# Kernel optimization log

Measured on AMD Instinct MI355X. Metric: run time of the kernel, lower is better.

The kernel has to match this reference:

```python
import jax, jax.numpy as jnp
import numpy as np
import math

M = 4096   # mem_dim == hidden_size (required: C @ qt)
D = 2048   # input_size


def setup_inputs() -> dict:
    key = jax.random.key(0)
    ks = jax.random.split(key, 16)
    f = lambda k, s: jax.random.normal(k, s, dtype=jnp.float32)
    return {
        "x": f(ks[0], (D, 1)),
        "cp": f(ks[1], (M, M)),
        "n_prev": f(ks[2], (M, 1)),
        "Wq": f(ks[3], (M, D)),
        "bq": f(ks[4], (M, 1)),
        "Wk": f(ks[5], (M, D)),
        "bk": f(ks[6], (M, 1)),
        "Wv": f(ks[7], (M, D)),
        "bV": f(ks[8], (M, 1)),
        "Wi": f(ks[9], (1, D)),
        "bi": f(ks[10], (1,)),
        "Wf": f(ks[11], (1, D)),
        "bf": f(ks[12], (1,)),
        "Wo": f(ks[13], (1, D)),
        "bo": f(ks[14], (1,)),
    }


def reference(x, cp, n_prev, Wq, bq, Wk, bk, Wv, bV, Wi, bi, Wf, bf, Wo, bo):
    inv_sqrt_m = 1.0 / math.sqrt(M)
    qt = Wq @ x + bq                      # (M, 1)
    kt = inv_sqrt_m * (Wk @ x + bk)       # (M, 1)
    vt = Wv @ x + bV                      # (M, 1)
    it = jnp.exp(Wi @ x + bi)             # (1, 1) input gate (exp)
    ft = jnp.exp(Wf @ x + bf)             # (1, 1) forget gate (exp)
    v = vt[:, 0]                          # (M,)
    k = kt[:, 0]                          # (M,)
    # matrix memory update: C = f*C_prev + i * v k^T
    C = ft * cp + it * jnp.outer(v, k)    # (M, M)
    n = ft * n_prev + it * k[:, None]     # (M, 1)
    denom = jnp.maximum(jnp.abs(n.T @ qt), 1.0)   # (1, 1)
    h_tilde = (C @ qt) / denom            # (M, 1)
    ot = jax.nn.sigmoid(Wo @ x + bo)      # (1, 1)
    ht = ot * h_tilde                     # (M, 1)
    return (ht, C, n)
```

## Files before the change

kernel.cpp:

```cpp
#include <hip/hip_runtime.h>
#include <math.h>

#define MM 4096
#define DD 2048

typedef float floatx4 __attribute__((ext_vector_type(4)));


__global__ __launch_bounds__(256) void k1_gemv_gates(
    const float* __restrict__ x,
    const float* __restrict__ Wq, const float* __restrict__ bq,
    const float* __restrict__ Wk, const float* __restrict__ bk,
    const float* __restrict__ Wv, const float* __restrict__ bV,
    const float* __restrict__ Wi, const float* __restrict__ bi,
    const float* __restrict__ Wf, const float* __restrict__ bf,
    const float* __restrict__ Wo, const float* __restrict__ bo,
    float* __restrict__ ws)
{
    const int lane = threadIdx.x & 63;
    const int wid  = threadIdx.x >> 6;

    if (blockIdx.x >= 3072) {
        __shared__ double gred[4];
        const int g = blockIdx.x - 3072;
        const float* G = (g == 0) ? Wi : ((g == 1) ? Wf : Wo);
        const float4* g4 = (const float4*)G;
        const float4* xv = (const float4*)x;
        double acc = 0.0;
        for (int t = threadIdx.x; t < DD / 4; t += 256) {
            float4 gg = g4[t];
            float4 xx = xv[t];
            acc += (double)gg.x * xx.x + (double)gg.y * xx.y
                 + (double)gg.z * xx.z + (double)gg.w * xx.w;
        }
        for (int off = 32; off; off >>= 1) acc += __shfl_down(acc, off, 64);
        if (lane == 0) gred[wid] = acc;
        __syncthreads();
        if (threadIdx.x == 0) {
            double s = gred[0] + gred[1] + gred[2] + gred[3];
            if (g == 0)      ws[3 * MM + 0] = (float)exp(s + (double)bi[0]);
            else if (g == 1) ws[3 * MM + 1] = (float)exp(s + (double)bf[0]);
            else             ws[3 * MM + 2] = (float)(1.0 / (1.0 + exp(-(s + (double)bo[0]))));
        }
        return;
    }

    __shared__ float xs[DD];

    {
        const float4* xv  = (const float4*)x;
        float4*       xsv = (float4*)xs;
        xsv[threadIdx.x]       = xv[threadIdx.x];
        xsv[256 + threadIdx.x] = xv[256 + threadIdx.x];
    }
    __syncthreads();

    const int m   = blockIdx.x >> 10;
    const int row = ((blockIdx.x & 1023) << 2) + wid;

    const float* W = (m == 0) ? Wq : ((m == 1) ? Wk : Wv);
    const float4* w4  = (const float4*)(W + (size_t)row * DD);
    const float4* xs4 = (const float4*)xs;

    float acc = 0.f;
    #pragma unroll
    for (int t = 0; t < DD / 4 / 64; ++t) {
        float4 ww = w4 [t * 64 + lane];
        float4 xx = xs4[t * 64 + lane];
        acc += ww.x * xx.x + ww.y * xx.y + ww.z * xx.z + ww.w * xx.w;
    }

    for (int off = 32; off; off >>= 1) acc += __shfl_down(acc, off, 64);

    if (lane == 0) {
        if (m == 0)      ws[row]          = acc + bq[row];
        else if (m == 1) ws[MM + row]     = (acc + bk[row]) * (1.0f / 64.0f);
        else             ws[2 * MM + row] = acc + bV[row];
    }
}

__global__ __launch_bounds__(256) void k2_rowC(
    const float* __restrict__ cp, const float* __restrict__ n_prev,
    float* __restrict__ ws, float* __restrict__ C_out, float* __restrict__ n_out)
{
    const int lane = threadIdx.x & 63;
    const int wid  = threadIdx.x >> 6;

    if (blockIdx.x == MM) {
        __shared__ float pred[4];
        const float it = ws[3 * MM + 0];
        const float ft = ws[3 * MM + 1];
        const float4* np4 = (const float4*)n_prev;
        const float4* kv4 = (const float4*)(ws + MM);
        const float4* qv4 = (const float4*)ws;
        float4* n4 = (float4*)n_out;
        float acc = 0.f;
        #pragma unroll
        for (int u = 0; u < 4; ++u) {
            int t = threadIdx.x + 256 * u;
            float4 np = np4[t], kk = kv4[t], qq = qv4[t];
            float4 nn;
            nn.x = fmaf(ft, np.x, it * kk.x);
            nn.y = fmaf(ft, np.y, it * kk.y);
            nn.z = fmaf(ft, np.z, it * kk.z);
            nn.w = fmaf(ft, np.w, it * kk.w);
            n4[t] = nn;
            acc += nn.x * qq.x + nn.y * qq.y + nn.z * qq.z + nn.w * qq.w;
        }
        for (int off = 32; off; off >>= 1) acc += __shfl_down(acc, off, 64);
        if (lane == 0) pred[wid] = acc;
        __syncthreads();
        if (threadIdx.x == 0) {
            float s = pred[0] + pred[1] + pred[2] + pred[3];
            ws[3 * MM + 3] = fmaxf(fabsf(s), 1.0f);
        }
        return;
    }

    __shared__ float sred[4];
    const int row = blockIdx.x;
    const float it  = ws[3 * MM + 0];
    const float ft  = ws[3 * MM + 1];
    const float ivi = it * ws[2 * MM + row];

    const float4* cprow = (const float4*)(cp + (size_t)row * MM);
    const float4* kv4   = (const float4*)(ws + MM);
    const float4* qv4   = (const float4*)ws;
    float4*       crow  = (float4*)(C_out + (size_t)row * MM);

    float4 c[4], kk[4], qq[4];
    #pragma unroll
    for (int u = 0; u < 4; ++u) c[u]  = cprow[threadIdx.x + 256 * u];
    #pragma unroll
    for (int u = 0; u < 4; ++u) kk[u] = kv4[threadIdx.x + 256 * u];
    #pragma unroll
    for (int u = 0; u < 4; ++u) qq[u] = qv4[threadIdx.x + 256 * u];

    float acc = 0.f;
    #pragma unroll
    for (int u = 0; u < 4; ++u) {
        float4 o;
        o.x = fmaf(ivi, kk[u].x, ft * c[u].x);
        o.y = fmaf(ivi, kk[u].y, ft * c[u].y);
        o.z = fmaf(ivi, kk[u].z, ft * c[u].z);
        o.w = fmaf(ivi, kk[u].w, ft * c[u].w);
        floatx4 ov = { o.x, o.y, o.z, o.w };
        __builtin_nontemporal_store(ov, (floatx4*)(crow + threadIdx.x + 256 * u));
        acc += o.x * qq[u].x + o.y * qq[u].y + o.z * qq[u].z + o.w * qq[u].w;
    }
    for (int off = 32; off; off >>= 1) acc += __shfl_down(acc, off, 64);
    if (lane == 0) sred[wid] = acc;
    __syncthreads();
    if (threadIdx.x == 0)
        ws[4 * MM + row] = sred[0] + sred[1] + sred[2] + sred[3];
}

__global__ __launch_bounds__(256) void k3_finalize(
    const float* __restrict__ ws, float* __restrict__ ht_out)
{
    const float ot    = ws[3 * MM + 2];
    const float denom = ws[3 * MM + 3];
    const int i = blockIdx.x * 256 + threadIdx.x;
    ht_out[i] = ot * (ws[4 * MM + i] / denom);
}

extern "C" void kernel_launch(void* const* d_in, const int* in_sizes, int n_in,
                              void* d_out, int out_size, void* d_ws, size_t ws_size,
                              hipStream_t stream)
{
    const float* x      = (const float*)d_in[0];
    const float* cp     = (const float*)d_in[1];
    const float* n_prev = (const float*)d_in[2];
    const float* Wq = (const float*)d_in[3];
    const float* bq = (const float*)d_in[4];
    const float* Wk = (const float*)d_in[5];
    const float* bk = (const float*)d_in[6];
    const float* Wv = (const float*)d_in[7];
    const float* bV = (const float*)d_in[8];
    const float* Wi = (const float*)d_in[9];
    const float* bi = (const float*)d_in[10];
    const float* Wf = (const float*)d_in[11];
    const float* bf = (const float*)d_in[12];
    const float* Wo = (const float*)d_in[13];
    const float* bo = (const float*)d_in[14];

    float* out = (float*)d_out;
    float* ht  = out;
    float* C   = out + MM;
    float* n   = out + MM + (size_t)MM * MM;
    float* ws  = (float*)d_ws;

    k1_gemv_gates<<<3075, 256, 0, stream>>>(x, Wq, bq, Wk, bk, Wv, bV,
                                            Wi, bi, Wf, bf, Wo, bo, ws);
    k2_rowC      <<<MM + 1, 256, 0, stream>>>(cp, n_prev, ws, C, n);
    k3_finalize  <<<MM / 256, 256, 0, stream>>>(ws, ht);
}
```

Baseline: 223.8 us.

## Process four C rows per block with k and q staged in shared memory

The row-update kernel now gives each wavefront its own row of C, so every block handles four rows and the grid shrinks from 4097 to 1025 blocks. The k and q vectors are loaded once per block into shared memory instead of being reread from global memory for every row. The block-level reduction and its barrier go away because each wave writes its own dot product. The cost is 32 KB of shared memory per block, which can limit occupancy, plus a barrier before the streaming loop.

```diff
diff --git a/kernel.cpp b/kernel.cpp
--- a/kernel.cpp
+++ b/kernel.cpp
@@ -86,7 +86,7 @@
     const int lane = threadIdx.x & 63;
     const int wid  = threadIdx.x >> 6;
 
-    if (blockIdx.x == MM) {
+    if (blockIdx.x == 1024) {
         __shared__ float pred[4];
         const float it = ws[3 * MM + 0];
         const float ft = ws[3 * MM + 1];
@@ -117,42 +117,44 @@
         return;
     }
 
-    __shared__ float sred[4];
-    const int row = blockIdx.x;
-    const float it  = ws[3 * MM + 0];
-    const float ft  = ws[3 * MM + 1];
+    __shared__ float4 kq[2][MM / 4];
+    const float it = ws[3 * MM + 0];
+    const float ft = ws[3 * MM + 1];
+
+    {
+        const float4* kv4 = (const float4*)(ws + MM);
+        const float4* qv4 = (const float4*)ws;
+        #pragma unroll
+        for (int u = 0; u < 4; ++u) kq[0][threadIdx.x + 256 * u] = kv4[threadIdx.x + 256 * u];
+        #pragma unroll
+        for (int u = 0; u < 4; ++u) kq[1][threadIdx.x + 256 * u] = qv4[threadIdx.x + 256 * u];
+    }
+    __syncthreads();
+
+    const int row = (blockIdx.x << 2) + wid;
     const float ivi = it * ws[2 * MM + row];
 
     const float4* cprow = (const float4*)(cp + (size_t)row * MM);
-    const float4* kv4   = (const float4*)(ws + MM);
-    const float4* qv4   = (const float4*)ws;
     float4*       crow  = (float4*)(C_out + (size_t)row * MM);
-
-    float4 c[4], kk[4], qq[4];
-    #pragma unroll
-    for (int u = 0; u < 4; ++u) c[u]  = cprow[threadIdx.x + 256 * u];
-    #pragma unroll
-    for (int u = 0; u < 4; ++u) kk[u] = kv4[threadIdx.x + 256 * u];
-    #pragma unroll
-    for (int u = 0; u < 4; ++u) qq[u] = qv4[threadIdx.x + 256 * u];
 
     float acc = 0.f;
     #pragma unroll
-    for (int u = 0; u < 4; ++u) {
+    for (int u = 0; u < 16; ++u) {
+        const int idx = lane + 64 * u;
+        float4 c  = cprow[idx];
+        float4 kk = kq[0][idx];
+        float4 qq = kq[1][idx];
         float4 o;
-        o.x = fmaf(ivi, kk[u].x, ft * c[u].x);
-        o.y = fmaf(ivi, kk[u].y, ft * c[u].y);
-        o.z = fmaf(ivi, kk[u].z, ft * c[u].z);
-        o.w = fmaf(ivi, kk[u].w, ft * c[u].w);
+        o.x = fmaf(ivi, kk.x, ft * c.x);
+        o.y = fmaf(ivi, kk.y, ft * c.y);
+        o.z = fmaf(ivi, kk.z, ft * c.z);
+        o.w = fmaf(ivi, kk.w, ft * c.w);
         floatx4 ov = { o.x, o.y, o.z, o.w };
-        __builtin_nontemporal_store(ov, (floatx4*)(crow + threadIdx.x + 256 * u));
-        acc += o.x * qq[u].x + o.y * qq[u].y + o.z * qq[u].z + o.w * qq[u].w;
+        __builtin_nontemporal_store(ov, (floatx4*)(crow + idx));
+        acc += o.x * qq.x + o.y * qq.y + o.z * qq.z + o.w * qq.w;
     }
     for (int off = 32; off; off >>= 1) acc += __shfl_down(acc, off, 64);
-    if (lane == 0) sred[wid] = acc;
-    __syncthreads();
-    if (threadIdx.x == 0)
-        ws[4 * MM + row] = sred[0] + sred[1] + sred[2] + sred[3];
+    if (lane == 0) ws[4 * MM + row] = acc;
 }
 
 __global__ __launch_bounds__(256) void k3_finalize(
@@ -192,6 +194,6 @@
 
     k1_gemv_gates<<<3075, 256, 0, stream>>>(x, Wq, bq, Wk, bk, Wv, bV,
                                             Wi, bi, Wf, bf, Wo, bo, ws);
-    k2_rowC      <<<MM + 1, 256, 0, stream>>>(cp, n_prev, ws, C, n);
+    k2_rowC      <<<1025, 256, 0, stream>>>(cp, n_prev, ws, C, n);
     k3_finalize  <<<MM / 256, 256, 0, stream>>>(ws, ht);
 }
```

Measured after the change: 223.8 us. About the same (+0.0%).
